# Performance work log

Measured on AMD Instinct MI355X. Metric: run time of the kernel, lower is better.

Reference implementation:

```python
import jax, jax.numpy as jnp
import numpy as np

NUM_CLASSES = 100
TEMPERATURE = 0.7
EPS = 1e-8  # F.cosine_similarity default eps
N, D = 8192, 256


def setup_inputs() -> dict:
    key = jax.random.key(0)
    k1, k2 = jax.random.split(key)
    fusion_feature = jax.random.normal(k1, (N, D), dtype=jnp.float32)
    labels = jax.random.randint(k2, (N,), 0, NUM_CLASSES, dtype=jnp.int64)
    return {"fusion_feature": fusion_feature, "labels": labels}


def reference(fusion_feature, labels):
    n = fusion_feature.shape[0]
    # --- label-grouped mean prototypes (scatter-mean by label) ---
    sums = jax.ops.segment_sum(fusion_feature, labels, num_segments=NUM_CLASSES)
    counts = jax.ops.segment_sum(jnp.ones((n,), fusion_feature.dtype), labels,
                                 num_segments=NUM_CLASSES)
    proto = sums / jnp.maximum(counts, 1.0)[:, None]   # [C, D]
    u = proto[labels]                                   # [n, D] prototype per sample
    # --- cosine similarity matrix [n, n] (torch eps-clamped norms) ---
    f_norm = jnp.maximum(jnp.linalg.norm(fusion_feature, axis=1), EPS)  # [n]
    u_norm = jnp.maximum(jnp.linalg.norm(u, axis=1), EPS)               # [n]
    sim = (fusion_feature @ u.T) / (f_norm[:, None] * u_norm[None, :])  # [n, n]
    # --- contrastive reduction ---
    e = jnp.exp(sim / TEMPERATURE)
    row_sum = jnp.sum(e, axis=1)          # denominator over all prototypes
    diag = jnp.diagonal(e)                # numerator: own prototype
    loss = jnp.sum(-jnp.log(diag / row_sum)) / n
    return loss
```

## Files before the change

### kernel.cpp

```cpp
#include <hip/hip_runtime.h>
#include <hip/hip_bf16.h>

#define NROWS 8192
#define DIM 256
#define NCLS 100
#define NCLS_PAD 128
#define TEMP 0.7f
#define EPSV 1e-8f
#define LMAX 512

typedef __attribute__((ext_vector_type(8))) short short8;
typedef __attribute__((ext_vector_type(4))) float f32x4;

static __device__ __forceinline__ short f2bf(float x) {
    union { float f; unsigned u; } c; c.f = x;
    unsigned r = (c.u + 0x7FFFu + ((c.u >> 16) & 1u)) >> 16;
    return (short)r;
}

__global__ __launch_bounds__(256) void k_proto(const float* __restrict__ f,
                                               const int* __restrict__ labels,
                                               unsigned short* __restrict__ protoB,
                                               float* __restrict__ countf,
                                               float* __restrict__ out) {
    int c = blockIdx.x, tid = threadIdx.x;
    __shared__ int list[LMAX];
    __shared__ int nm;
    __shared__ float4 red4[256];
    if (tid == 0) nm = 0;
    __syncthreads();
    #pragma unroll
    for (int i = 0; i < NROWS / 256; ++i) {
        int r = i * 256 + tid;
        if (labels[r] == c) {
            int idx = atomicAdd(&nm, 1);
            if (idx < LMAX) list[idx] = r;
        }
    }
    __syncthreads();
    int n = nm < LMAX ? nm : LMAX;
    int g = tid >> 6, d = tid & 63;
    float4 acc = make_float4(0.f, 0.f, 0.f, 0.f);
    int i = g;
    for (; i + 16 <= n; i += 16) {
        float4 v0 = *(const float4*)&f[list[i + 0] * DIM + d * 4];
        float4 v1 = *(const float4*)&f[list[i + 4] * DIM + d * 4];
        float4 v2 = *(const float4*)&f[list[i + 8] * DIM + d * 4];
        float4 v3 = *(const float4*)&f[list[i + 12] * DIM + d * 4];
        acc.x += (v0.x + v1.x) + (v2.x + v3.x);
        acc.y += (v0.y + v1.y) + (v2.y + v3.y);
        acc.z += (v0.z + v1.z) + (v2.z + v3.z);
        acc.w += (v0.w + v1.w) + (v2.w + v3.w);
    }
    for (; i < n; i += 4) {
        float4 v = *(const float4*)&f[list[i] * DIM + d * 4];
        acc.x += v.x; acc.y += v.y; acc.z += v.z; acc.w += v.w;
    }
    red4[tid] = acc;
    __syncthreads();
    if (tid < 64) {
        float4 a0 = red4[d], a1 = red4[d + 64], a2 = red4[d + 128], a3 = red4[d + 192];
        float invn = 1.0f / fmaxf((float)n, 1.0f);
        float mx = (a0.x + a1.x + a2.x + a3.x) * invn;
        float my = (a0.y + a1.y + a2.y + a3.y) * invn;
        float mz = (a0.z + a1.z + a2.z + a3.z) * invn;
        float mw = (a0.w + a1.w + a2.w + a3.w) * invn;
        float ssq = mx * mx + my * my + mz * mz + mw * mw;
        #pragma unroll
        for (int m = 32; m > 0; m >>= 1) ssq += __shfl_xor(ssq, m);
        float scale = 1.0f / (fmaxf(sqrtf(ssq), EPSV) * TEMP);
        ushort4 o;
        o.x = (unsigned short)f2bf(mx * scale);
        o.y = (unsigned short)f2bf(my * scale);
        o.z = (unsigned short)f2bf(mz * scale);
        o.w = (unsigned short)f2bf(mw * scale);
        *(ushort4*)&protoB[c * DIM + d * 4] = o;
        if (d == 0) {
            countf[c] = (float)n;
            if (c == NCLS_PAD - 1) out[0] = 0.0f;
        }
    }
}

__global__ __launch_bounds__(64) void k_main(const float* __restrict__ f,
                                             const int* __restrict__ labels,
                                             const unsigned short* __restrict__ protoB,
                                             const float* __restrict__ countf,
                                             float* __restrict__ out) {
    int l   = threadIdx.x;
    int rb  = blockIdx.x * 16;
    int n16 = l & 15, q = l >> 4;
    __shared__ float invfS[16];
    __shared__ float dgS[16];

    f32x4 acc[8];
    #pragma unroll
    for (int t = 0; t < 8; ++t) acc[t] = (f32x4){0.f, 0.f, 0.f, 0.f};

    const float* arow = f + (rb + n16) * DIM + q * 8;
    float ss = 0.0f;

    #pragma unroll
    for (int kc = 0; kc < DIM; kc += 32) {
        float4 a0 = *(const float4*)(arow + kc);
        float4 a1 = *(const float4*)(arow + kc + 4);
        ss += a0.x * a0.x + a0.y * a0.y + a0.z * a0.z + a0.w * a0.w;
        ss += a1.x * a1.x + a1.y * a1.y + a1.z * a1.z + a1.w * a1.w;
        short8 af;
        af[0] = f2bf(a0.x); af[1] = f2bf(a0.y); af[2] = f2bf(a0.z); af[3] = f2bf(a0.w);
        af[4] = f2bf(a1.x); af[5] = f2bf(a1.y); af[6] = f2bf(a1.z); af[7] = f2bf(a1.w);
        short8 bf[8];
        #pragma unroll
        for (int t = 0; t < 8; ++t)
            bf[t] = *(const short8*)&protoB[(t * 16 + n16) * DIM + kc + q * 8];
        #pragma unroll
        for (int t = 0; t < 8; ++t)
            acc[t] = __builtin_amdgcn_mfma_f32_16x16x32_bf16(af, bf[t], acc[t], 0, 0, 0);
    }

    ss += __shfl_xor(ss, 16);
    ss += __shfl_xor(ss, 32);
    if (q == 0) invfS[n16] = 1.0f / fmaxf(sqrtf(ss), EPSV);
    __syncthreads();

    int lab[4];
    float inv4[4];
    #pragma unroll
    for (int j = 0; j < 4; ++j) {
        lab[j]  = labels[rb + q * 4 + j];
        inv4[j] = invfS[q * 4 + j];
    }
    float rp[4] = {0.f, 0.f, 0.f, 0.f};
    #pragma unroll
    for (int t = 0; t < 8; ++t) {
        int col   = n16 + 16 * t;
        float cfv = countf[col];
        #pragma unroll
        for (int j = 0; j < 4; ++j) {
            float a = acc[t][j] * inv4[j];
            rp[j] += cfv * __expf(a);
            if (col == lab[j]) dgS[q * 4 + j] = a;
        }
    }
    __syncthreads();
    #pragma unroll
    for (int m = 1; m <= 8; m <<= 1) {
        #pragma unroll
        for (int j = 0; j < 4; ++j) rp[j] += __shfl_xor(rp[j], m);
    }
    float lsum = 0.0f;
    #pragma unroll
    for (int j = 0; j < 4; ++j) lsum += __logf(rp[j]) - dgS[q * 4 + j];
    float contrib = (n16 == 0) ? lsum : 0.0f;
    contrib += __shfl_xor(contrib, 16);
    contrib += __shfl_xor(contrib, 32);
    if (l == 0) atomicAdd(out, contrib * (1.0f / (float)NROWS));
}

extern "C" void kernel_launch(void* const* d_in, const int* in_sizes, int n_in,
                              void* d_out, int out_size, void* d_ws, size_t ws_size,
                              hipStream_t stream) {
    const float* f      = (const float*)d_in[0];
    const int*   labels = (const int*)d_in[1];
    unsigned short* protoB = (unsigned short*)d_ws;
    float* countf          = (float*)d_ws + 16384;

    k_proto<<<NCLS_PAD, 256, 0, stream>>>(f, labels, protoB, countf, (float*)d_out);
    k_main<<<NROWS / 16, 64, 0, stream>>>(f, labels, protoB, countf, (float*)d_out);
}
```

Before: 86.27 us.

## Split main kernel across four waves with LDS-staged bf16 rows; widen prototype kernel

k_main now runs 256 threads per 16-row block. The block cooperatively converts the fp32 feature rows to bf16 in swizzled LDS and computes the row norms. Each of the four waves then covers two 16-column prototype tiles instead of one wave doing all eight, with row sums combined through shared memory before the atomic. k_proto doubles to 512 threads and preloads the labels into registers so more memory loads are in flight during the gather. The aim is more parallelism per block and less per-wave serial MFMA and exp work, at the cost of an extra LDS round trip and a barrier.

After: 74.98 us. 13.1% less time.

```diff
diff --git a/kernel.cpp b/kernel.cpp
--- a/kernel.cpp
+++ b/kernel.cpp
@@ -1,5 +1,4 @@
 #include <hip/hip_runtime.h>
-#include <hip/hip_bf16.h>
 
 #define NROWS 8192
 #define DIM 256
@@ -12,13 +11,12 @@
 typedef __attribute__((ext_vector_type(8))) short short8;
 typedef __attribute__((ext_vector_type(4))) float f32x4;
 
-static __device__ __forceinline__ short f2bf(float x) {
-    union { float f; unsigned u; } c; c.f = x;
-    unsigned r = (c.u + 0x7FFFu + ((c.u >> 16) & 1u)) >> 16;
-    return (short)r;
+static __device__ __forceinline__ unsigned short f2bf(float x) {
+    unsigned u = __builtin_bit_cast(unsigned, x);
+    return (unsigned short)((u + 0x7FFFu + ((u >> 16) & 1u)) >> 16);
 }
 
-__global__ __launch_bounds__(256) void k_proto(const float* __restrict__ f,
+__global__ __launch_bounds__(512) void k_proto(const float* __restrict__ f,
                                                const int* __restrict__ labels,
                                                unsigned short* __restrict__ protoB,
                                                float* __restrict__ countf,
@@ -26,54 +24,63 @@
     int c = blockIdx.x, tid = threadIdx.x;
     __shared__ int list[LMAX];
     __shared__ int nm;
-    __shared__ float4 red4[256];
+    __shared__ float4 red4[512];
     if (tid == 0) nm = 0;
     __syncthreads();
+    int lv[16];
     #pragma unroll
-    for (int i = 0; i < NROWS / 256; ++i) {
-        int r = i * 256 + tid;
-        if (labels[r] == c) {
+    for (int i = 0; i < 16; ++i) lv[i] = labels[i * 512 + tid];
+    #pragma unroll
+    for (int i = 0; i < 16; ++i)
+        if (lv[i] == c) {
             int idx = atomicAdd(&nm, 1);
-            if (idx < LMAX) list[idx] = r;
+            if (idx < LMAX) list[idx] = i * 512 + tid;
         }
-    }
     __syncthreads();
     int n = nm < LMAX ? nm : LMAX;
     int g = tid >> 6, d = tid & 63;
     float4 acc = make_float4(0.f, 0.f, 0.f, 0.f);
     int i = g;
-    for (; i + 16 <= n; i += 16) {
-        float4 v0 = *(const float4*)&f[list[i + 0] * DIM + d * 4];
-        float4 v1 = *(const float4*)&f[list[i + 4] * DIM + d * 4];
-        float4 v2 = *(const float4*)&f[list[i + 8] * DIM + d * 4];
-        float4 v3 = *(const float4*)&f[list[i + 12] * DIM + d * 4];
+    for (; i + 32 <= n; i += 32) {
+        float4 v0 = *(const float4*)&f[list[i +  0] * DIM + d * 4];
+        float4 v1 = *(const float4*)&f[list[i +  8] * DIM + d * 4];
+        float4 v2 = *(const float4*)&f[list[i + 16] * DIM + d * 4];
+        float4 v3 = *(const float4*)&f[list[i + 24] * DIM + d * 4];
         acc.x += (v0.x + v1.x) + (v2.x + v3.x);
         acc.y += (v0.y + v1.y) + (v2.y + v3.y);
         acc.z += (v0.z + v1.z) + (v2.z + v3.z);
         acc.w += (v0.w + v1.w) + (v2.w + v3.w);
     }
-    for (; i < n; i += 4) {
+    for (; i + 16 <= n; i += 16) {
+        float4 v0 = *(const float4*)&f[list[i + 0] * DIM + d * 4];
+        float4 v1 = *(const float4*)&f[list[i + 8] * DIM + d * 4];
+        acc.x += v0.x + v1.x; acc.y += v0.y + v1.y;
+        acc.z += v0.z + v1.z; acc.w += v0.w + v1.w;
+    }
+    for (; i < n; i += 8) {
         float4 v = *(const float4*)&f[list[i] * DIM + d * 4];
         acc.x += v.x; acc.y += v.y; acc.z += v.z; acc.w += v.w;
     }
     red4[tid] = acc;
     __syncthreads();
     if (tid < 64) {
-        float4 a0 = red4[d], a1 = red4[d + 64], a2 = red4[d + 128], a3 = red4[d + 192];
+        float4 s = red4[d];
+        #pragma unroll
+        for (int k = 1; k < 8; ++k) {
+            float4 t = red4[d + 64 * k];
+            s.x += t.x; s.y += t.y; s.z += t.z; s.w += t.w;
+        }
         float invn = 1.0f / fmaxf((float)n, 1.0f);
-        float mx = (a0.x + a1.x + a2.x + a3.x) * invn;
-        float my = (a0.y + a1.y + a2.y + a3.y) * invn;
-        float mz = (a0.z + a1.z + a2.z + a3.z) * invn;
-        float mw = (a0.w + a1.w + a2.w + a3.w) * invn;
+        float mx = s.x * invn, my = s.y * invn, mz = s.z * invn, mw = s.w * invn;
         float ssq = mx * mx + my * my + mz * mz + mw * mw;
         #pragma unroll
         for (int m = 32; m > 0; m >>= 1) ssq += __shfl_xor(ssq, m);
         float scale = 1.0f / (fmaxf(sqrtf(ssq), EPSV) * TEMP);
         ushort4 o;
-        o.x = (unsigned short)f2bf(mx * scale);
-        o.y = (unsigned short)f2bf(my * scale);
-        o.z = (unsigned short)f2bf(mz * scale);
-        o.w = (unsigned short)f2bf(mw * scale);
+        o.x = f2bf(mx * scale);
+        o.y = f2bf(my * scale);
+        o.z = f2bf(mz * scale);
+        o.w = f2bf(mw * scale);
         *(ushort4*)&protoB[c * DIM + d * 4] = o;
         if (d == 0) {
             countf[c] = (float)n;
@@ -82,79 +89,92 @@
     }
 }
 
-__global__ __launch_bounds__(64) void k_main(const float* __restrict__ f,
-                                             const int* __restrict__ labels,
-                                             const unsigned short* __restrict__ protoB,
-                                             const float* __restrict__ countf,
-                                             float* __restrict__ out) {
-    int l   = threadIdx.x;
-    int rb  = blockIdx.x * 16;
-    int n16 = l & 15, q = l >> 4;
+__global__ __launch_bounds__(256) void k_main(const float* __restrict__ f,
+                                              const int* __restrict__ labels,
+                                              const unsigned short* __restrict__ protoB,
+                                              const float* __restrict__ countf,
+                                              float* __restrict__ out) {
+    int tid = threadIdx.x;
+    int rb = blockIdx.x * 16;
+    __shared__ unsigned short As[16 * DIM];
     __shared__ float invfS[16];
     __shared__ float dgS[16];
+    __shared__ float wsum[4][16];
+    char* asb = (char*)As;
 
-    f32x4 acc[8];
-    #pragma unroll
-    for (int t = 0; t < 8; ++t) acc[t] = (f32x4){0.f, 0.f, 0.f, 0.f};
+    {
+        int row = tid >> 4, s = tid & 15;
+        const float* fr = f + (rb + row) * DIM;
+        float4 v[4];
+        #pragma unroll
+        for (int i = 0; i < 4; ++i) v[i] = *(const float4*)(fr + (s + 16 * i) * 4);
+        float ss = 0.f;
+        #pragma unroll
+        for (int i = 0; i < 4; ++i) {
+            ss += v[i].x * v[i].x + v[i].y * v[i].y + v[i].z * v[i].z + v[i].w * v[i].w;
+            ushort4 o;
+            o.x = f2bf(v[i].x); o.y = f2bf(v[i].y); o.z = f2bf(v[i].z); o.w = f2bf(v[i].w);
+            int byte = (row * 512 + s * 8 + i * 128) ^ ((row & 7) << 4);
+            *(ushort4*)(asb + byte) = o;
+        }
+        ss += __shfl_xor(ss, 1); ss += __shfl_xor(ss, 2);
+        ss += __shfl_xor(ss, 4); ss += __shfl_xor(ss, 8);
+        if (s == 0) invfS[row] = 1.0f / fmaxf(sqrtf(ss), EPSV);
+    }
+    __syncthreads();
 
-    const float* arow = f + (rb + n16) * DIM + q * 8;
-    float ss = 0.0f;
-
+    int w = tid >> 6, l = tid & 63;
+    int n16 = l & 15, q = l >> 4;
+    f32x4 acc0 = {0.f, 0.f, 0.f, 0.f}, acc1 = {0.f, 0.f, 0.f, 0.f};
+    const unsigned short* pb0 = protoB + ((2 * w)     * 16 + n16) * DIM + q * 8;
+    const unsigned short* pb1 = protoB + ((2 * w + 1) * 16 + n16) * DIM + q * 8;
+    int arow = n16 * 512 + q * 16;
+    int swz  = (n16 & 7) << 4;
     #pragma unroll
     for (int kc = 0; kc < DIM; kc += 32) {
-        float4 a0 = *(const float4*)(arow + kc);
-        float4 a1 = *(const float4*)(arow + kc + 4);
-        ss += a0.x * a0.x + a0.y * a0.y + a0.z * a0.z + a0.w * a0.w;
-        ss += a1.x * a1.x + a1.y * a1.y + a1.z * a1.z + a1.w * a1.w;
-        short8 af;
-        af[0] = f2bf(a0.x); af[1] = f2bf(a0.y); af[2] = f2bf(a0.z); af[3] = f2bf(a0.w);
-        af[4] = f2bf(a1.x); af[5] = f2bf(a1.y); af[6] = f2bf(a1.z); af[7] = f2bf(a1.w);
-        short8 bf[8];
-        #pragma unroll
-        for (int t = 0; t < 8; ++t)
-            bf[t] = *(const short8*)&protoB[(t * 16 + n16) * DIM + kc + q * 8];
-        #pragma unroll
-        for (int t = 0; t < 8; ++t)
-            acc[t] = __builtin_amdgcn_mfma_f32_16x16x32_bf16(af, bf[t], acc[t], 0, 0, 0);
+        short8 af = *(const short8*)(asb + ((arow + kc * 2) ^ swz));
+        short8 b0 = *(const short8*)(pb0 + kc);
+        short8 b1 = *(const short8*)(pb1 + kc);
+        acc0 = __builtin_amdgcn_mfma_f32_16x16x32_bf16(af, b0, acc0, 0, 0, 0);
+        acc1 = __builtin_amdgcn_mfma_f32_16x16x32_bf16(af, b1, acc1, 0, 0, 0);
     }
 
-    ss += __shfl_xor(ss, 16);
-    ss += __shfl_xor(ss, 32);
-    if (q == 0) invfS[n16] = 1.0f / fmaxf(sqrtf(ss), EPSV);
-    __syncthreads();
-
-    int lab[4];
+    int lab4[4];
     float inv4[4];
     #pragma unroll
     for (int j = 0; j < 4; ++j) {
-        lab[j]  = labels[rb + q * 4 + j];
+        lab4[j] = labels[rb + q * 4 + j];
         inv4[j] = invfS[q * 4 + j];
     }
-    float rp[4] = {0.f, 0.f, 0.f, 0.f};
+    int col0 = n16 + 16 * (2 * w);
+    int col1 = col0 + 16;
+    float cf0 = countf[col0], cf1 = countf[col1];
+    float rp[4];
     #pragma unroll
-    for (int t = 0; t < 8; ++t) {
-        int col   = n16 + 16 * t;
-        float cfv = countf[col];
-        #pragma unroll
-        for (int j = 0; j < 4; ++j) {
-            float a = acc[t][j] * inv4[j];
-            rp[j] += cfv * __expf(a);
-            if (col == lab[j]) dgS[q * 4 + j] = a;
-        }
+    for (int j = 0; j < 4; ++j) {
+        float a0 = acc0[j] * inv4[j];
+        float a1 = acc1[j] * inv4[j];
+        rp[j] = cf0 * __expf(a0) + cf1 * __expf(a1);
+        if (col0 == lab4[j]) dgS[q * 4 + j] = a0;
+        if (col1 == lab4[j]) dgS[q * 4 + j] = a1;
     }
-    __syncthreads();
     #pragma unroll
     for (int m = 1; m <= 8; m <<= 1) {
         #pragma unroll
         for (int j = 0; j < 4; ++j) rp[j] += __shfl_xor(rp[j], m);
     }
-    float lsum = 0.0f;
-    #pragma unroll
-    for (int j = 0; j < 4; ++j) lsum += __logf(rp[j]) - dgS[q * 4 + j];
-    float contrib = (n16 == 0) ? lsum : 0.0f;
-    contrib += __shfl_xor(contrib, 16);
-    contrib += __shfl_xor(contrib, 32);
-    if (l == 0) atomicAdd(out, contrib * (1.0f / (float)NROWS));
+    if (n16 == 0) {
+        #pragma unroll
+        for (int j = 0; j < 4; ++j) wsum[w][q * 4 + j] = rp[j];
+    }
+    __syncthreads();
+    if (tid < 16) {
+        float tot = wsum[0][tid] + wsum[1][tid] + wsum[2][tid] + wsum[3][tid];
+        float v = __logf(tot) - dgS[tid];
+        v += __shfl_xor(v, 1); v += __shfl_xor(v, 2);
+        v += __shfl_xor(v, 4); v += __shfl_xor(v, 8);
+        if (tid == 0) atomicAdd(out, v * (1.0f / (float)NROWS));
+    }
 }
 
 extern "C" void kernel_launch(void* const* d_in, const int* in_sizes, int n_in,
@@ -165,6 +185,6 @@
     unsigned short* protoB = (unsigned short*)d_ws;
     float* countf          = (float*)d_ws + 16384;
 
-    k_proto<<<NCLS_PAD, 256, 0, stream>>>(f, labels, protoB, countf, (float*)d_out);
-    k_main<<<NROWS / 16, 64, 0, stream>>>(f, labels, protoB, countf, (float*)d_out);
+    k_proto<<<NCLS_PAD, 512, 0, stream>>>(f, labels, protoB, countf, (float*)d_out);
+    k_main<<<NROWS / 16, 256, 0, stream>>>(f, labels, protoB, countf, (float*)d_out);
 }
```
